# Optimization experiments

Hardware: AMD Instinct MI355X
Metric: run time of the kernel (lower is better)

The kernel has to match this reference:

```python
import jax, jax.numpy as jnp
import numpy as np
from jax import lax


def build_edges(M, K):
    # star edges keypoint<->root per instrument, plus bidirectional clique over roots
    edges = []
    for m in range(M):
        base = m * K
        root = base + (K - 1)
        for kp in range(K - 1):
            u = base + kp
            edges.append((u, root))
            edges.append((root, u))
    roots = [m * K + (K - 1) for m in range(M)]
    for i in range(len(roots)):
        for j in range(i + 1, len(roots)):
            edges.append((roots[i], roots[j]))
            edges.append((roots[j], roots[i]))
    e = np.asarray(edges, dtype=np.int32).T  # (2, E)
    return jnp.asarray(e[0]), jnp.asarray(e[1])


def lstm(xs, w_ih, w_hh, b_ih, b_hh):
    # xs: (T, BN, in); torch gate order i, f, g, o
    H = w_hh.shape[1]
    BN = xs.shape[1]
    h0 = jnp.zeros((BN, H), xs.dtype)
    c0 = jnp.zeros((BN, H), xs.dtype)

    def step(carry, x):
        h, c = carry
        g = x @ w_ih.T + b_ih + h @ w_hh.T + b_hh
        i, f, gg, o = jnp.split(g, 4, axis=-1)
        c = jax.nn.sigmoid(f) * c + jax.nn.sigmoid(i) * jnp.tanh(gg)
        h = jax.nn.sigmoid(o) * jnp.tanh(c)
        return (h, c), h

    _, hs = lax.scan(step, (h0, c0), xs)
    return hs  # (T, BN, H)


def gat_layer(x, W, a, b, src, dst, N):
    # x: (N, H_in); single-head GAT with LeakyReLU(0.2) scores, ELU output
    h = x @ W                                   # (N, O)
    O = W.shape[1]
    a_src, a_dst = a[:O], a[O:]
    e = jax.nn.leaky_relu(h[src] @ a_src + h[dst] @ a_dst, 0.2)  # (E,)
    emax = jax.ops.segment_max(e, dst, num_segments=N)
    ex = jnp.exp(e - emax[dst])
    denom = jax.ops.segment_sum(ex, dst, num_segments=N)
    alpha = ex / denom[dst]
    out = jax.ops.segment_sum(alpha[:, None] * h[src], dst, num_segments=N) + b
    return jax.nn.elu(out)


def setup_inputs() -> dict:
    key = jax.random.key(0)
    ks = jax.random.split(key, 24)
    B, T, M, K = 64, 128, 8, 5
    E, H = 16, 32
    s = 0.1
    d = {
        'feat': jax.random.uniform(ks[0], (B, T, M, K, 3), jnp.float32),
        'phi_w1': jax.random.normal(ks[1], (3, E)) * s,
        'phi_b1': jax.random.normal(ks[2], (E,)) * s,
        'phi_w2': jax.random.normal(ks[3], (E, E)) * s,
        'phi_b2': jax.random.normal(ks[4], (E,)) * s,
        'spa_wih': jax.random.normal(ks[5], (4 * H, E)) * s,
        'spa_whh': jax.random.normal(ks[6], (4 * H, H)) * s,
        'spa_bih': jax.random.normal(ks[7], (4 * H,)) * s,
        'spa_bhh': jax.random.normal(ks[8], (4 * H,)) * s,
        'bn_gamma': jnp.ones((H,)),
        'bn_beta': jnp.zeros((H,)),
        'gat1_w': jax.random.normal(ks[9], (H, H)) * s,
        'gat1_a': jax.random.normal(ks[10], (2 * H,)) * s,
        'gat1_b': jnp.zeros((H,)),
        'gat2_w': jax.random.normal(ks[11], (H, H)) * s,
        'gat2_a': jax.random.normal(ks[12], (2 * H,)) * s,
        'gat2_b': jnp.zeros((H,)),
        'temp_wih': jax.random.normal(ks[13], (4 * H, H)) * s,
        'temp_whh': jax.random.normal(ks[14], (4 * H, H)) * s,
        'temp_bih': jax.random.normal(ks[15], (4 * H,)) * s,
        'temp_bhh': jax.random.normal(ks[16], (4 * H,)) * s,
    }
    return d


def reference(feat, phi_w1, phi_b1, phi_w2, phi_b2,
              spa_wih, spa_whh, spa_bih, spa_bhh,
              bn_gamma, bn_beta,
              gat1_w, gat1_a, gat1_b, gat2_w, gat2_a, gat2_b,
              temp_wih, temp_whh, temp_bih, temp_bhh):
    B, T, M, K, _ = feat.shape
    # --- add_virtual_root ---
    xy = feat[..., :2]
    vis = feat[..., 2] > 0.5
    w = vis[..., None].astype(feat.dtype)
    denom = jnp.clip(w.sum(axis=3, keepdims=True), 1.0, None)
    root_xy = (xy * w).sum(axis=3, keepdims=True) / denom
    root_vis = jnp.any(vis, axis=3, keepdims=True).astype(feat.dtype)[..., None]
    featR = jnp.concatenate([feat, jnp.concatenate([root_xy, root_vis], -1)], axis=3)
    KR = K + 1
    N = M * KR
    # --- phi MLP ---
    v = jax.nn.relu(featR @ phi_w1 + phi_b1) @ phi_w2 + phi_b2  # (B,T,M,KR,E)
    v = v.reshape(B, T, N, -1)
    # --- spatial LSTM over T, batch B*N ---
    xs = v.transpose(1, 0, 2, 3).reshape(T, B * N, -1)
    H = spa_whh.shape[1]
    r = lstm(xs, spa_wih, spa_whh, spa_bih, spa_bhh).reshape(T, B, N, H).transpose(1, 0, 2, 3)
    # --- per-timestep BatchNorm (training-mode batch stats over B*N) ---
    def bn_t(x_t):  # (B,N,H)
        xf = x_t.reshape(-1, H)
        mu = xf.mean(0)
        var = ((xf - mu) ** 2).mean(0)
        return (x_t - mu) / jnp.sqrt(var + 1e-5) * bn_gamma + bn_beta
    x_bn = jax.vmap(bn_t, in_axes=1, out_axes=1)(r)  # (B,T,N,H)
    # --- two GAT layers per (b,t) graph ---
    src, dst = build_edges(M, KR)
    xflat = x_bn.reshape(B * T, N, H)
    g1 = jax.vmap(lambda z: gat_layer(z, gat1_w, gat1_a, gat1_b, src, dst, N))(xflat)
    g2 = jax.vmap(lambda z: gat_layer(z, gat2_w, gat2_a, gat2_b, src, dst, N))(g1)
    rhat = g2.reshape(B, T, N, H)
    # --- temporal LSTM ---
    temp_in = rhat.transpose(1, 0, 2, 3).reshape(T, B * N, H)
    l = lstm(temp_in, temp_wih, temp_whh, temp_bih, temp_bhh).reshape(T, B, N, H).transpose(1, 0, 2, 3)
    h = jnp.concatenate([r, l], axis=-1)  # (B,T,N,2H)
    return (r, h)
```

## Files before the change

### kernel.cpp

```cpp
#include <hip/hip_runtime.h>

constexpr int B = 64, T = 128, M = 8, KLEAF = 5, KR = 6, N = 48, E = 16, H = 32;
constexpr int BNR = B * N;
constexpr int NG  = B * T;
constexpr int BNP = 16;
constexpr long long R_SIZE = (long long)B * T * N * H;

#define DEVI __device__ __forceinline__

DEVI float frcp(float x) { return __builtin_amdgcn_rcpf(x); }
DEVI float sigm(float x) { return frcp(1.f + __expf(-x)); }
DEVI float tanh_(float x) {
  float a = __expf(2.f * fabsf(x));
  float r = 1.f - 2.f * frcp(a + 1.f);
  return x >= 0.f ? r : -r;
}

__global__ __launch_bounds__(256) void k_phi(
    const float* __restrict__ feat, const float* __restrict__ w1,
    const float* __restrict__ b1, const float* __restrict__ w2,
    const float* __restrict__ b2, float* __restrict__ v_ws)
{
  int gid = blockIdx.x * 256 + threadIdx.x;
  if (gid >= B * T * N) return;
  int nn = gid % N;
  int bt = gid / N;
  int m = nn / KR, k = nn % KR;
  int t = bt % T, b = bt / T;
  const float* fp = feat + ((size_t)bt * M + m) * (KLEAF * 3);
  float x0, x1, x2;
  if (k < KLEAF) {
    x0 = fp[k * 3 + 0]; x1 = fp[k * 3 + 1]; x2 = fp[k * 3 + 2];
  } else {
    float sx = 0.f, sy = 0.f, sw = 0.f, av = 0.f;
#pragma unroll
    for (int kp = 0; kp < KLEAF; kp++) {
      float fx = fp[kp * 3], fy = fp[kp * 3 + 1], fv = fp[kp * 3 + 2];
      float w = fv > 0.5f ? 1.f : 0.f;
      sx += fx * w; sy += fy * w; sw += w; av = fmaxf(av, w);
    }
    float dn = fmaxf(sw, 1.f);
    x0 = sx / dn; x1 = sy / dn; x2 = av;
  }
  float hd[E];
#pragma unroll
  for (int e = 0; e < E; e++) {
    float v = b1[e] + x0 * w1[0 * E + e] + x1 * w1[1 * E + e] + x2 * w1[2 * E + e];
    hd[e] = v > 0.f ? v : 0.f;
  }
  float* vo = v_ws + ((size_t)t * BNR + (size_t)b * N + nn) * E;
#pragma unroll
  for (int e2 = 0; e2 < E; e2++) {
    float acc = b2[e2];
#pragma unroll
    for (int e = 0; e < E; e++) acc += hd[e] * w2[e * E + e2];
    vo[e2] = acc;
  }
}

template <int EE, int MODE>
__global__ __launch_bounds__(256) void k_lstm(
    const float* __restrict__ x, const float* __restrict__ wih,
    const float* __restrict__ whh, const float* __restrict__ bih,
    const float* __restrict__ bhh, float* __restrict__ dout)
{
  constexpr int X4 = EE / 4;
  int tid = threadIdx.x;
  int wave = tid >> 6;
  int pr_ = wave >> 1;
  int wsel = wave & 1;
  int lane = tid & 63;
  int j = lane & 31, hi = lane >> 5;
  int row = blockIdx.x * 2 + pr_;
  int b = row / N, n = row % N;
  int gate = wsel * 64 + hi * 32 + j;

  float Wx[EE], Wh[32];
#pragma unroll
  for (int e = 0; e < EE; e++) Wx[e] = wih[gate * EE + e];
#pragma unroll
  for (int k = 0; k < 32; k++) Wh[k] = whh[gate * 32 + k];
  float bs = bih[gate] + bhh[gate];

  __shared__ __align__(16) float hl[4][32];
  __shared__ __align__(16) float xl[2][2][EE];
  __shared__ float gx[2][2][2][2][32];

  if (hi == 0) hl[wave][j] = 0.f;
  const float* xrow = x + (size_t)row * EE;
  constexpr size_t XST = (size_t)BNR * EE;
  if (wsel == 0 && lane < X4)
    ((float4*)xl[pr_][0])[lane] = ((const float4*)xrow)[lane];
  __syncthreads();

  float c = 0.f;
  float* prp = dout + ((size_t)b * T * N + n) * H + j;
  float* php = dout + R_SIZE + ((size_t)b * T * N + n) * 2 * H + (MODE == 1 ? H : 0) + j;

  for (int t = 0; t < T; t++) {
    int par = t & 1;
    float4 xnv = {0, 0, 0, 0};
    int tn = t + 1 < T ? t + 1 : t;
    if (wsel == 0 && lane < X4)
      xnv = ((const float4*)(xrow + (size_t)tn * XST))[lane];
    float a0 = bs, a1 = 0.f, a2 = 0.f, a3 = 0.f;
    const float4* xp4 = (const float4*)xl[pr_][par];
#pragma unroll
    for (int q = 0; q < X4; q++) {
      float4 xv = xp4[q];
      a0 += Wx[4 * q + 0] * xv.x; a1 += Wx[4 * q + 1] * xv.y;
      a2 += Wx[4 * q + 2] * xv.z; a3 += Wx[4 * q + 3] * xv.w;
    }
    const float4* hp4 = (const float4*)hl[wave];
#pragma unroll
    for (int q = 0; q < 8; q++) {
      float4 hv = hp4[q];
      a0 += Wh[4 * q + 0] * hv.x; a1 += Wh[4 * q + 1] * hv.y;
      a2 += Wh[4 * q + 2] * hv.z; a3 += Wh[4 * q + 3] * hv.w;
    }
    float a = (a0 + a1) + (a2 + a3);
    float act = (wsel == 0) ? sigm(a) : (hi ? sigm(a) : tanh_(a));
    gx[pr_][par][wsel][hi][j] = act;
    if (wsel == 0 && lane < X4)
      ((float4*)xl[pr_][par ^ 1])[lane] = xnv;
    __syncthreads();
    if (hi == 0) {
      float iv = gx[pr_][par][0][0][j];
      float fv = gx[pr_][par][0][1][j];
      float gv = gx[pr_][par][1][0][j];
      float ov = gx[pr_][par][1][1][j];
      c = fv * c + iv * gv;
      float hnew = ov * tanh_(c);
      hl[wave][j] = hnew;
      if (wsel == 0) {
        if (MODE == 0) { *prp = hnew; *php = hnew; }
        else { *php = hnew; }
      }
    }
    prp += N * H; php += N * 2 * H;
  }
}

__global__ __launch_bounds__(256) void k_bn1(
    const float* __restrict__ r, float* __restrict__ part)
{
  int t = blockIdx.x, p = blockIdx.y;
  int c = threadIdx.x & 31, rg = threadIdx.x >> 5;
  constexpr int RPP = BNR / BNP;
  float s = 0.f, s2 = 0.f;
  for (int row = p * RPP + rg; row < (p + 1) * RPP; row += 8) {
    int b = row / N, n = row % N;
    float x = r[((size_t)b * T + t) * N * H + (size_t)n * H + c];
    s += x; s2 += x * x;
  }
  __shared__ float sm[2][8][32];
  sm[0][rg][c] = s; sm[1][rg][c] = s2;
  __syncthreads();
  if (rg == 0) {
    float ss = 0.f, ss2 = 0.f;
#pragma unroll
    for (int i = 0; i < 8; i++) { ss += sm[0][i][c]; ss2 += sm[1][i][c]; }
    part[((size_t)t * BNP + p) * 64 + c] = ss;
    part[((size_t)t * BNP + p) * 64 + 32 + c] = ss2;
  }
}

__global__ void k_bn2(
    const float* __restrict__ part, const float* __restrict__ gamma,
    const float* __restrict__ beta, float* __restrict__ sctab)
{
  int t = blockIdx.x, c = threadIdx.x;
  float ss = 0.f, ss2 = 0.f;
#pragma unroll
  for (int p = 0; p < BNP; p++) {
    ss  += part[((size_t)t * BNP + p) * 64 + c];
    ss2 += part[((size_t)t * BNP + p) * 64 + 32 + c];
  }
  float mu = ss * (1.f / BNR);
  float var = ss2 * (1.f / BNR) - mu * mu;
  float rstd = rsqrtf(var + 1e-5f);
  float sc = gamma[c] * rstd;
  sctab[t * 64 + c] = sc;
  sctab[t * 64 + 32 + c] = beta[c] - mu * sc;
}

__global__ __launch_bounds__(256) void k_gat(
    const float* __restrict__ r, const float* __restrict__ sctab,
    const float* __restrict__ w1, const float* __restrict__ a1, const float* __restrict__ bg1,
    const float* __restrict__ w2, const float* __restrict__ a2, const float* __restrict__ bg2,
    float* __restrict__ gat_ws)
{
  int g = blockIdx.x;
  int b = g >> 7, t = g & 127;
  int tid = threadIdx.x;
  __shared__ float X[N][H];
  __shared__ float Hm[N][H + 1];
  __shared__ float Wl[H * H];
  __shared__ float ssrc[N], sdst[N];
  __shared__ float alph[M][12];
  for (int i = tid; i < N * H; i += 256) {
    int cc = i & 31;
    ((float*)X)[i] = r[(size_t)g * N * H + i] * sctab[t * 64 + cc] + sctab[t * 64 + 32 + cc];
  }
  const float* Ws[2] = {w1, w2};
  const float* As[2] = {a1, a2};
  const float* Bs[2] = {bg1, bg2};
  int oc = tid & 31, n0 = tid >> 5;
  for (int layer = 0; layer < 2; layer++) {
    const float* av = As[layer];
    const float* bias = Bs[layer];
    for (int i = tid; i < H * H; i += 256) Wl[i] = Ws[layer][i];
    __syncthreads();
#pragma unroll
    for (int rep = 0; rep < 6; rep++) {
      int n = n0 + rep * 8;
      float acc = 0.f;
#pragma unroll
      for (int kk = 0; kk < H; kk++) acc += X[n][kk] * Wl[kk * H + oc];
      Hm[n][oc] = acc;
    }
    __syncthreads();
    if (tid < N) {
      float as = 0.f, ad = 0.f;
#pragma unroll
      for (int kk = 0; kk < H; kk++) {
        float x = Hm[tid][kk];
        as += x * av[kk]; ad += x * av[H + kk];
      }
      ssrc[tid] = as; sdst[tid] = ad;
    }
    __syncthreads();
    if (tid < M) {
      float ev[12];
      float sd = sdst[tid * KR + KR - 1];
#pragma unroll
      for (int kp = 0; kp < KLEAF; kp++) ev[kp] = ssrc[tid * KR + kp] + sd;
#pragma unroll
      for (int j = 0; j < 7; j++) {
        int mm = j < tid ? j : j + 1;
        ev[KLEAF + j] = ssrc[mm * KR + KR - 1] + sd;
      }
      float mx = -1e30f;
#pragma unroll
      for (int i = 0; i < 12; i++) {
        float e = ev[i]; e = e > 0.f ? e : 0.2f * e;
        ev[i] = e; mx = fmaxf(mx, e);
      }
      float s = 0.f;
#pragma unroll
      for (int i = 0; i < 12; i++) { float e = __expf(ev[i] - mx); ev[i] = e; s += e; }
      float inv = frcp(s);
#pragma unroll
      for (int i = 0; i < 12; i++) alph[tid][i] = ev[i] * inv;
    }
    __syncthreads();
    float hv[6];
#pragma unroll
    for (int rep = 0; rep < 6; rep++) {
      int n = n0 + rep * 8;
      int m2 = n / KR;
      float acc;
      if (n % KR == KR - 1) {
        acc = 0.f;
#pragma unroll
        for (int kp = 0; kp < KLEAF; kp++) acc += alph[m2][kp] * Hm[m2 * KR + kp][oc];
#pragma unroll
        for (int j = 0; j < 7; j++) {
          int mm = j < m2 ? j : j + 1;
          acc += alph[m2][KLEAF + j] * Hm[mm * KR + KR - 1][oc];
        }
      } else {
        acc = Hm[m2 * KR + KR - 1][oc];
      }
      acc += bias[oc];
      hv[rep] = acc > 0.f ? acc : __expf(acc) - 1.f;
    }
    __syncthreads();
#pragma unroll
    for (int rep = 0; rep < 6; rep++) X[n0 + rep * 8][oc] = hv[rep];
    __syncthreads();
  }
  for (int i = tid; i < N * H; i += 256)
    gat_ws[((size_t)t * BNR + (size_t)b * N) * H + i] = ((float*)X)[i];
}

extern "C" void kernel_launch(void* const* d_in, const int* in_sizes, int n_in,
                              void* d_out, int out_size, void* d_ws, size_t ws_size,
                              hipStream_t stream)
{
  const float* feat     = (const float*)d_in[0];
  const float* phi_w1   = (const float*)d_in[1];
  const float* phi_b1   = (const float*)d_in[2];
  const float* phi_w2   = (const float*)d_in[3];
  const float* phi_b2   = (const float*)d_in[4];
  const float* spa_wih  = (const float*)d_in[5];
  const float* spa_whh  = (const float*)d_in[6];
  const float* spa_bih  = (const float*)d_in[7];
  const float* spa_bhh  = (const float*)d_in[8];
  const float* bn_gamma = (const float*)d_in[9];
  const float* bn_beta  = (const float*)d_in[10];
  const float* gat1_w   = (const float*)d_in[11];
  const float* gat1_a   = (const float*)d_in[12];
  const float* gat1_b   = (const float*)d_in[13];
  const float* gat2_w   = (const float*)d_in[14];
  const float* gat2_a   = (const float*)d_in[15];
  const float* gat2_b   = (const float*)d_in[16];
  const float* temp_wih = (const float*)d_in[17];
  const float* temp_whh = (const float*)d_in[18];
  const float* temp_bih = (const float*)d_in[19];
  const float* temp_bhh = (const float*)d_in[20];
  float* out = (float*)d_out;

  float* v_ws   = (float*)d_ws;
  float* gat_ws = v_ws   + (size_t)T * BNR * E;
  float* bnpart = gat_ws + (size_t)T * BNR * H;
  float* sctab  = bnpart + (size_t)T * BNP * 64;

  k_phi <<<(B * T * N + 255) / 256, 256, 0, stream>>>(feat, phi_w1, phi_b1, phi_w2, phi_b2, v_ws);
  k_lstm<16, 0><<<BNR / 2, 256, 0, stream>>>(v_ws, spa_wih, spa_whh, spa_bih, spa_bhh, out);
  k_bn1 <<<dim3(T, BNP), 256, 0, stream>>>(out, bnpart);
  k_bn2 <<<T, 32, 0, stream>>>(bnpart, bn_gamma, bn_beta, sctab);
  k_gat <<<NG, 256, 0, stream>>>(out, sctab, gat1_w, gat1_a, gat1_b, gat2_w, gat2_a, gat2_b, gat_ws);
  k_lstm<32, 1><<<BNR / 2, 256, 0, stream>>>(gat_ws, temp_wih, temp_whh, temp_bih, temp_bhh, out);
}
```

Before: 521.2 us.

## Precompute LSTM input projections in producer kernels, drop per-step x@Wih from recurrence

The input-to-gate projection (x @ W_ih^T) for both LSTMs is moved out of the sequential recurrence and fused into the producing kernels (k_phi for the spatial LSTM, k_gat for the temporal LSTM). Those kernels write a 128-wide gate preactivation per row, and each LSTM thread then loads a single scalar per step. This shortens the per-step critical path and frees the Wx registers. The cost is a larger workspace (128 floats per row instead of 16 or 32) and more global write and read traffic. Launch bounds are also tightened to raise occupancy.

```diff
diff --git a/kernel.cpp b/kernel.cpp
--- a/kernel.cpp
+++ b/kernel.cpp
@@ -16,13 +16,19 @@
   return x >= 0.f ? r : -r;
 }
 
-__global__ __launch_bounds__(256) void k_phi(
+__global__ __launch_bounds__(256, 4) void k_phi(
     const float* __restrict__ feat, const float* __restrict__ w1,
     const float* __restrict__ b1, const float* __restrict__ w2,
-    const float* __restrict__ b2, float* __restrict__ v_ws)
-{
-  int gid = blockIdx.x * 256 + threadIdx.x;
-  if (gid >= B * T * N) return;
+    const float* __restrict__ b2, const float* __restrict__ wih,
+    float* __restrict__ xw)
+{
+  __shared__ float wT[E][128];
+  int tid = threadIdx.x;
+  for (int i = tid; i < E * 128; i += 256) {
+    int e = i >> 7, g = i & 127;
+    wT[e][g] = wih[g * E + e];
+  }
+  int gid = blockIdx.x * 256 + tid;
   int nn = gid % N;
   int bt = gid / N;
   int m = nn / KR, k = nn % KR;
@@ -48,23 +54,42 @@
     float v = b1[e] + x0 * w1[0 * E + e] + x1 * w1[1 * E + e] + x2 * w1[2 * E + e];
     hd[e] = v > 0.f ? v : 0.f;
   }
-  float* vo = v_ws + ((size_t)t * BNR + (size_t)b * N + nn) * E;
+  float vv[E];
 #pragma unroll
   for (int e2 = 0; e2 < E; e2++) {
     float acc = b2[e2];
 #pragma unroll
     for (int e = 0; e < E; e++) acc += hd[e] * w2[e * E + e2];
-    vo[e2] = acc;
-  }
-}
-
-template <int EE, int MODE>
-__global__ __launch_bounds__(256) void k_lstm(
-    const float* __restrict__ x, const float* __restrict__ wih,
-    const float* __restrict__ whh, const float* __restrict__ bih,
-    const float* __restrict__ bhh, float* __restrict__ dout)
-{
-  constexpr int X4 = EE / 4;
+    vv[e2] = acc;
+  }
+  __syncthreads();
+  float* xo = xw + ((size_t)t * BNR + b * N + nn) * 128;
+  for (int pass = 0; pass < 4; pass++) {
+    float4 a4[8];
+#pragma unroll
+    for (int c = 0; c < 8; c++) a4[c] = make_float4(0.f, 0.f, 0.f, 0.f);
+#pragma unroll
+    for (int e = 0; e < E; e++) {
+      float ve = vv[e];
+      const float4* wr = (const float4*)&wT[e][pass * 32];
+#pragma unroll
+      for (int c = 0; c < 8; c++) {
+        float4 w4 = wr[c];
+        a4[c].x += ve * w4.x; a4[c].y += ve * w4.y;
+        a4[c].z += ve * w4.z; a4[c].w += ve * w4.w;
+      }
+    }
+#pragma unroll
+    for (int c = 0; c < 8; c++) ((float4*)xo)[pass * 8 + c] = a4[c];
+  }
+}
+
+template <int MODE>
+__global__ __launch_bounds__(256, 6) void k_lstm(
+    const float* __restrict__ xw, const float* __restrict__ whh,
+    const float* __restrict__ bih, const float* __restrict__ bhh,
+    float* __restrict__ dout)
+{
   int tid = threadIdx.x;
   int wave = tid >> 6;
   int pr_ = wave >> 1;
@@ -75,23 +100,18 @@
   int b = row / N, n = row % N;
   int gate = wsel * 64 + hi * 32 + j;
 
-  float Wx[EE], Wh[32];
-#pragma unroll
-  for (int e = 0; e < EE; e++) Wx[e] = wih[gate * EE + e];
+  float Wh[32];
 #pragma unroll
   for (int k = 0; k < 32; k++) Wh[k] = whh[gate * 32 + k];
   float bs = bih[gate] + bhh[gate];
 
   __shared__ __align__(16) float hl[4][32];
-  __shared__ __align__(16) float xl[2][2][EE];
   __shared__ float gx[2][2][2][2][32];
-
   if (hi == 0) hl[wave][j] = 0.f;
-  const float* xrow = x + (size_t)row * EE;
-  constexpr size_t XST = (size_t)BNR * EE;
-  if (wsel == 0 && lane < X4)
-    ((float4*)xl[pr_][0])[lane] = ((const float4*)xrow)[lane];
-  __syncthreads();
+
+  const float* xpt = xw + (size_t)row * 128 + gate;
+  float xc = *xpt;
+  xpt += (size_t)BNR * 128;
 
   float c = 0.f;
   float* prp = dout + ((size_t)b * T * N + n) * H + j;
@@ -99,18 +119,9 @@
 
   for (int t = 0; t < T; t++) {
     int par = t & 1;
-    float4 xnv = {0, 0, 0, 0};
-    int tn = t + 1 < T ? t + 1 : t;
-    if (wsel == 0 && lane < X4)
-      xnv = ((const float4*)(xrow + (size_t)tn * XST))[lane];
-    float a0 = bs, a1 = 0.f, a2 = 0.f, a3 = 0.f;
-    const float4* xp4 = (const float4*)xl[pr_][par];
-#pragma unroll
-    for (int q = 0; q < X4; q++) {
-      float4 xv = xp4[q];
-      a0 += Wx[4 * q + 0] * xv.x; a1 += Wx[4 * q + 1] * xv.y;
-      a2 += Wx[4 * q + 2] * xv.z; a3 += Wx[4 * q + 3] * xv.w;
-    }
+    float xn = 0.f;
+    if (t < T - 1) { xn = *xpt; xpt += (size_t)BNR * 128; }
+    float a0 = bs + xc, a1 = 0.f, a2 = 0.f, a3 = 0.f;
     const float4* hp4 = (const float4*)hl[wave];
 #pragma unroll
     for (int q = 0; q < 8; q++) {
@@ -121,8 +132,6 @@
     float a = (a0 + a1) + (a2 + a3);
     float act = (wsel == 0) ? sigm(a) : (hi ? sigm(a) : tanh_(a));
     gx[pr_][par][wsel][hi][j] = act;
-    if (wsel == 0 && lane < X4)
-      ((float4*)xl[pr_][par ^ 1])[lane] = xnv;
     __syncthreads();
     if (hi == 0) {
       float iv = gx[pr_][par][0][0][j];
@@ -137,6 +146,7 @@
         else { *php = hnew; }
       }
     }
+    xc = xn;
     prp += N * H; php += N * 2 * H;
   }
 }
@@ -184,11 +194,11 @@
   sctab[t * 64 + 32 + c] = beta[c] - mu * sc;
 }
 
-__global__ __launch_bounds__(256) void k_gat(
+__global__ __launch_bounds__(256, 4) void k_gat(
     const float* __restrict__ r, const float* __restrict__ sctab,
     const float* __restrict__ w1, const float* __restrict__ a1, const float* __restrict__ bg1,
     const float* __restrict__ w2, const float* __restrict__ a2, const float* __restrict__ bg2,
-    float* __restrict__ gat_ws)
+    const float* __restrict__ twih, float* __restrict__ xw)
 {
   int g = blockIdx.x;
   int b = g >> 7, t = g & 127;
@@ -196,11 +206,16 @@
   __shared__ float X[N][H];
   __shared__ float Hm[N][H + 1];
   __shared__ float Wl[H * H];
+  __shared__ float wT2[H][128];
   __shared__ float ssrc[N], sdst[N];
   __shared__ float alph[M][12];
   for (int i = tid; i < N * H; i += 256) {
     int cc = i & 31;
     ((float*)X)[i] = r[(size_t)g * N * H + i] * sctab[t * 64 + cc] + sctab[t * 64 + 32 + cc];
+  }
+  for (int i = tid; i < H * 128; i += 256) {
+    int k = i >> 7, gg = i & 127;
+    wT2[k][gg] = twih[gg * H + k];
   }
   const float* Ws[2] = {w1, w2};
   const float* As[2] = {a1, a2};
@@ -280,8 +295,36 @@
     for (int rep = 0; rep < 6; rep++) X[n0 + rep * 8][oc] = hv[rep];
     __syncthreads();
   }
-  for (int i = tid; i < N * H; i += 256)
-    gat_ws[((size_t)t * BNR + (size_t)b * N) * H + i] = ((float*)X)[i];
+  int g4 = tid & 31;
+  int nb = tid >> 5;
+  float4 acc[6];
+#pragma unroll
+  for (int rp = 0; rp < 6; rp++) acc[rp] = make_float4(0.f, 0.f, 0.f, 0.f);
+  for (int kc = 0; kc < 4; kc++) {
+    float4 w4r[8];
+#pragma unroll
+    for (int k8 = 0; k8 < 8; k8++) w4r[k8] = ((const float4*)wT2[kc * 8 + k8])[g4];
+#pragma unroll
+    for (int rp = 0; rp < 6; rp++) {
+      int nn2 = rp * 8 + nb;
+      float4 xa = ((const float4*)X[nn2])[kc * 2 + 0];
+      float4 xb = ((const float4*)X[nn2])[kc * 2 + 1];
+      acc[rp].x += xa.x * w4r[0].x + xa.y * w4r[1].x + xa.z * w4r[2].x + xa.w * w4r[3].x
+                 + xb.x * w4r[4].x + xb.y * w4r[5].x + xb.z * w4r[6].x + xb.w * w4r[7].x;
+      acc[rp].y += xa.x * w4r[0].y + xa.y * w4r[1].y + xa.z * w4r[2].y + xa.w * w4r[3].y
+                 + xb.x * w4r[4].y + xb.y * w4r[5].y + xb.z * w4r[6].y + xb.w * w4r[7].y;
+      acc[rp].z += xa.x * w4r[0].z + xa.y * w4r[1].z + xa.z * w4r[2].z + xa.w * w4r[3].z
+                 + xb.x * w4r[4].z + xb.y * w4r[5].z + xb.z * w4r[6].z + xb.w * w4r[7].z;
+      acc[rp].w += xa.x * w4r[0].w + xa.y * w4r[1].w + xa.z * w4r[2].w + xa.w * w4r[3].w
+                 + xb.x * w4r[4].w + xb.y * w4r[5].w + xb.z * w4r[6].w + xb.w * w4r[7].w;
+    }
+  }
+  float* xo = xw + ((size_t)t * BNR + b * N) * 128;
+#pragma unroll
+  for (int rp = 0; rp < 6; rp++) {
+    int nn2 = rp * 8 + nb;
+    ((float4*)(xo + nn2 * 128))[g4] = acc[rp];
+  }
 }
 
 extern "C" void kernel_launch(void* const* d_in, const int* in_sizes, int n_in,
@@ -311,15 +354,14 @@
   const float* temp_bhh = (const float*)d_in[20];
   float* out = (float*)d_out;
 
-  float* v_ws   = (float*)d_ws;
-  float* gat_ws = v_ws   + (size_t)T * BNR * E;
-  float* bnpart = gat_ws + (size_t)T * BNR * H;
+  float* xw     = (float*)d_ws;
+  float* bnpart = xw + (size_t)T * BNR * 128;
   float* sctab  = bnpart + (size_t)T * BNP * 64;
 
-  k_phi <<<(B * T * N + 255) / 256, 256, 0, stream>>>(feat, phi_w1, phi_b1, phi_w2, phi_b2, v_ws);
-  k_lstm<16, 0><<<BNR / 2, 256, 0, stream>>>(v_ws, spa_wih, spa_whh, spa_bih, spa_bhh, out);
+  k_phi <<<(B * T * N) / 256, 256, 0, stream>>>(feat, phi_w1, phi_b1, phi_w2, phi_b2, spa_wih, xw);
+  k_lstm<0><<<BNR / 2, 256, 0, stream>>>(xw, spa_whh, spa_bih, spa_bhh, out);
   k_bn1 <<<dim3(T, BNP), 256, 0, stream>>>(out, bnpart);
   k_bn2 <<<T, 32, 0, stream>>>(bnpart, bn_gamma, bn_beta, sctab);
-  k_gat <<<NG, 256, 0, stream>>>(out, sctab, gat1_w, gat1_a, gat1_b, gat2_w, gat2_a, gat2_b, gat_ws);
-  k_lstm<32, 1><<<BNR / 2, 256, 0, stream>>>(gat_ws, temp_wih, temp_whh, temp_bih, temp_bhh, out);
-}
+  k_gat <<<NG, 256, 0, stream>>>(out, sctab, gat1_w, gat1_a, gat1_b, gat2_w, gat2_a, gat2_b, temp_wih, xw);
+  k_lstm<1><<<BNR / 2, 256, 0, stream>>>(xw, temp_whh, temp_bih, temp_bhh, out);
+}
```

Result: slower. 756.2 us (+45.1%).
